# Kernel optimization log

Hardware: AMD Instinct MI355X
Metric: run time of the kernel (lower is better)

## Reference

```python
import jax, jax.numpy as jnp
import numpy as np

B, S, I, H = 32, 2048, 256, 256


def setup_inputs() -> dict:
    key = jax.random.key(0)
    ks = jax.random.split(key, 12)
    scale = 1.0 / np.sqrt(H + I)  # torch Linear default init scale-ish
    def w(k):
        return jax.random.normal(k, (H + I, H), dtype=jnp.float32) * scale
    def b(k):
        return jax.random.normal(k, (H,), dtype=jnp.float32) * scale
    return {
        "x": jax.random.normal(ks[0], (B, S, I), dtype=jnp.float32),
        "h0": jax.random.normal(ks[1], (1, B, H), dtype=jnp.float32),
        "c0": jax.random.normal(ks[2], (1, B, H), dtype=jnp.float32),
        "Wf": w(ks[3]), "bf": b(ks[4]),
        "Wi": w(ks[5]), "bi": b(ks[6]),
        "Wc": w(ks[7]), "bc": b(ks[8]),
        "Wo": w(ks[9]), "bo": b(ks[10]),
    }


def reference(x, h0, c0, Wf, bf, Wi, bi, Wc, bc, Wo, bo):
    # Fuse the four gate GEMMs into one: W_all [H+I, 4H], b_all [4H]
    W_all = jnp.concatenate([Wf, Wi, Wc, Wo], axis=1)
    b_all = jnp.concatenate([bf, bi, bc, bo], axis=0)
    Hh = h0.shape[-1]

    def step(carry, x_t):
        h, c = carry  # [B,H]
        hx = jnp.concatenate([h, x_t], axis=-1)          # [B, H+I]
        g = hx @ W_all + b_all                            # [B, 4H]
        f = jax.nn.sigmoid(g[:, 0*Hh:1*Hh])
        i = jax.nn.sigmoid(g[:, 1*Hh:2*Hh])
        cand = jnp.tanh(g[:, 2*Hh:3*Hh])
        o = jax.nn.sigmoid(g[:, 3*Hh:4*Hh])
        c_new = c * f + i * cand
        h_new = o * jnp.tanh(c_new)
        return (h_new, c_new), h_new

    (h_f, c_f), hs = jax.lax.scan(step, (h0[0], c0[0]), jnp.swapaxes(x, 0, 1))
    hidden_states = jnp.swapaxes(hs, 0, 1)               # [B,S,H]
    return hidden_states, (h_f[None], c_f[None])
```

## Files before the change

### kernel.cpp

```cpp
#include <hip/hip_runtime.h>
#include <hip/hip_bf16.h>

typedef __attribute__((ext_vector_type(8))) short short8;
typedef __attribute__((ext_vector_type(4))) float floatx4;
typedef __attribute__((ext_vector_type(4))) unsigned int uintx4;
typedef unsigned int u32;

#define Bb 32
#define Ss 2048
#define Ii 256
#define Hh 256

#define DATA_OFF 4096
#define GX_OFF   65536
#define RETRY_DEAD (1u << 22)

__device__ __forceinline__ unsigned short f2bf(float f) {
    unsigned int u = __float_as_uint(f);
    u += 0x7fffu + ((u >> 16) & 1u);
    return (unsigned short)(u >> 16);
}
__device__ __forceinline__ float bf2f_lo(u32 w) { return __uint_as_float(w << 16); }
__device__ __forceinline__ float bf2f_hi(u32 w) { return __uint_as_float(w & 0xffff0000u); }

__device__ __forceinline__ float fast_sigmoid(float x) {
    return __builtin_amdgcn_rcpf(1.0f + __expf(-x));
}
__device__ __forceinline__ float fast_tanh(float x) {
    return 1.0f - 2.0f * __builtin_amdgcn_rcpf(__expf(2.0f * x) + 1.0f);
}

__device__ __forceinline__ void data_load8_s(const u32* pd, uintx4 v[8]) {
    asm volatile("global_load_dwordx4 %0, %8, off sc0 sc1\n\t"
                 "global_load_dwordx4 %1, %8, off offset:64 sc0 sc1\n\t"
                 "global_load_dwordx4 %2, %8, off offset:128 sc0 sc1\n\t"
                 "global_load_dwordx4 %3, %8, off offset:192 sc0 sc1\n\t"
                 "global_load_dwordx4 %4, %8, off offset:256 sc0 sc1\n\t"
                 "global_load_dwordx4 %5, %8, off offset:320 sc0 sc1\n\t"
                 "global_load_dwordx4 %6, %8, off offset:384 sc0 sc1\n\t"
                 "global_load_dwordx4 %7, %8, off offset:448 sc0 sc1\n\t"
                 "s_waitcnt vmcnt(0)"
                 : "=v"(v[0]), "=v"(v[1]), "=v"(v[2]), "=v"(v[3]),
                   "=v"(v[4]), "=v"(v[5]), "=v"(v[6]), "=v"(v[7])
                 : "v"(pd) : "memory");
}

__global__ __launch_bounds__(256, 2)
void lstm_gx_kernel(const float* __restrict__ x,
                    const float* __restrict__ Wf, const float* __restrict__ bfp,
                    const float* __restrict__ Wi, const float* __restrict__ bip,
                    const float* __restrict__ Wc, const float* __restrict__ bcp,
                    const float* __restrict__ Wo, const float* __restrict__ bop,
                    u32* __restrict__ gx)
{
    const int tid = threadIdx.x, wave = tid >> 6, lane = tid & 63;
    const int ln = lane & 15, lg = lane >> 4;
    const int combo = blockIdx.x & 7;
    const int tbase = (blockIdx.x >> 3) * 8;
    const int wg = ((combo & 1) << 2) + wave;
    const int chalf = (combo >> 1) & 1, mtile = combo >> 2;
    const int j0 = wg * 32 + chalf * 16, r0 = mtile * 16;
    const int wv = wg * 4 + chalf * 2 + mtile;

    const float* Wg[4] = {Wf, Wi, Wc, Wo};
    const float* bg[4] = {bfp, bip, bcp, bop};
    float bias[4];
#pragma unroll
    for (int g = 0; g < 4; ++g) bias[g] = bg[g][j0 + ln];

    short8 Bf[4][8];
#pragma unroll
    for (int g = 0; g < 4; ++g)
#pragma unroll
        for (int ks = 0; ks < 8; ++ks) {
            short8 v;
#pragma unroll
            for (int i = 0; i < 8; ++i) {
                int k = 256 + 32 * ks + 8 * lg + i;
                v[i] = (short)f2bf(Wg[g][k * Hh + (j0 + ln)]);
            }
            Bf[g][ks] = v;
        }

    for (int it = 0; it < 8; ++it) {
        int t = tbase + it;
        short8 xf[8];
#pragma unroll
        for (int ks = 0; ks < 8; ++ks) {
            const float* px = x + (r0 + ln) * (Ss * Ii) + t * Ii + 32 * ks + 8 * lg;
            floatx4 a = *(const floatx4*)px;
            floatx4 b = *(const floatx4*)(px + 4);
            short8 v;
#pragma unroll
            for (int q = 0; q < 4; ++q) { v[q] = (short)f2bf(a[q]); v[4 + q] = (short)f2bf(b[q]); }
            xf[ks] = v;
        }
        floatx4 acc[4];
#pragma unroll
        for (int g = 0; g < 4; ++g) acc[g] = (floatx4){0.f, 0.f, 0.f, 0.f};
#pragma unroll
        for (int ks = 0; ks < 8; ++ks)
#pragma unroll
            for (int g = 0; g < 4; ++g)
                acc[g] = __builtin_amdgcn_mfma_f32_16x16x32_bf16(xf[ks], Bf[g][ks], acc[g], 0, 0, 0);

        u32 o[8];
#pragma unroll
        for (int g = 0; g < 4; ++g)
#pragma unroll
            for (int rp = 0; rp < 2; ++rp) {
                float v0 = acc[g][2 * rp] + bias[g];
                float v1 = acc[g][2 * rp + 1] + bias[g];
                o[g * 2 + rp] = (u32)f2bf(v0) | ((u32)f2bf(v1) << 16);
            }
        u32* dst = gx + ((size_t)(t * 32 + wv) * 64 + lane) * 8;
        ((uintx4*)dst)[0] = (uintx4){o[0], o[1], o[2], o[3]};
        ((uintx4*)dst)[1] = (uintx4){o[4], o[5], o[6], o[7]};
    }
}

__global__ __launch_bounds__(256, 1)
void lstm_rec8(const float* __restrict__ h0,
               const float* __restrict__ c0,
               const float* __restrict__ Wf,
               const float* __restrict__ Wi,
               const float* __restrict__ Wc,
               const float* __restrict__ Wo,
               float* __restrict__ out,
               u32* data, const u32* __restrict__ gx)
{
    const int wg = blockIdx.x;
    const int tid = threadIdx.x;
    const int wave = tid >> 6, lane = tid & 63;
    const int mt = wave & 1, chalf = wave >> 1;
    const int ln = lane & 15, lg = lane >> 4;
    const int j0 = wg * 32 + chalf * 16;
    const int j = j0 + ln;
    const int wv = wg * 4 + chalf * 2 + mt;

    const float* Wg[4] = {Wf, Wi, Wc, Wo};
    short8 Bfrag[4][8];
#pragma unroll
    for (int g = 0; g < 4; ++g)
#pragma unroll
        for (int ks = 0; ks < 8; ++ks) {
            short8 v;
#pragma unroll
            for (int i = 0; i < 8; ++i) {
                int k = 32 * ks + 8 * lg + i;
                v[i] = (short)f2bf(Wg[g][k * Hh + j]);
            }
            Bfrag[g][ks] = v;
        }

    float cst[4], hl[4];
#pragma unroll
    for (int r = 0; r < 4; ++r) {
        cst[r] = c0[(16 * mt + 4 * lg + r) * Hh + j];
        hl[r] = 0.0f;
    }

    auto step_tail = [&](floatx4 (&acc)[4], int t, int sw_) {
        float hnew[4];
#pragma unroll
        for (int r = 0; r < 4; ++r) {
            float fg = fast_sigmoid(acc[0][r]);
            float ig = fast_sigmoid(acc[1][r]);
            float cd = fast_tanh(acc[2][r]);
            float og = fast_sigmoid(acc[3][r]);
            float c  = cst[r] * fg + ig * cd;
            cst[r] = c;
            hnew[r] = og * fast_tanh(c);
            hl[r] = hnew[r];
        }
        const u32 tb = 0x4000u | ((u32)(t & 1) << 30);
        u32 wrd[4];
#pragma unroll
        for (int r = 0; r < 4; ++r) {
            float partner = __shfl_xor(hnew[r], 1);
            wrd[r] = ((u32)f2bf(hnew[r]) | ((u32)f2bf(partner) << 16)) | tb;
        }
        u32* pw = data + sw_ * 4096 + (16 * mt + 4 * lg) * 128 + (j >> 1);
        if ((ln & 1) == 0) {
            asm volatile("global_store_dword %4, %0, off sc0 sc1\n\t"
                         "global_store_dword %4, %1, off offset:512 sc0 sc1\n\t"
                         "global_store_dword %4, %2, off offset:1024 sc0 sc1\n\t"
                         "global_store_dword %4, %3, off offset:1536 sc0 sc1"
                         :: "v"(wrd[0]), "v"(wrd[1]), "v"(wrd[2]), "v"(wrd[3]), "v"(pw)
                         : "memory");
        }
#pragma unroll
        for (int r = 0; r < 4; ++r)
            out[(16 * mt + 4 * lg + r) * (Ss * Hh) + t * Hh + j] = hnew[r];
    };

    auto run_mfma = [&](short8 (&afr)[8], floatx4 (&acc)[4]) {
#pragma unroll
        for (int ks = 0; ks < 8; ++ks)
#pragma unroll
            for (int g = 0; g < 4; ++g)
                acc[g] = __builtin_amdgcn_mfma_f32_16x16x32_bf16(afr[ks], Bfrag[g][ks], acc[g], 0, 0, 0);
    };

    uintx4 g0, g1;
    {
        const uintx4* p = (const uintx4*)(gx + ((size_t)wv * 64 + lane) * 8);
        g0 = p[0]; g1 = p[1];
    }

    {
        short8 a0[8];
        const float* hr = h0 + (16 * mt + ln) * Hh;
#pragma unroll
        for (int ks = 0; ks < 8; ++ks) {
            floatx4 a = *(const floatx4*)(hr + 32 * ks + 8 * lg);
            floatx4 b = *(const floatx4*)(hr + 32 * ks + 8 * lg + 4);
            short8 v;
#pragma unroll
            for (int q = 0; q < 4; ++q) { v[q] = (short)f2bf(a[q]); v[4 + q] = (short)f2bf(b[q]); }
            a0[ks] = v;
        }
        floatx4 acc[4];
        acc[0] = (floatx4){bf2f_lo(g0.x), bf2f_hi(g0.x), bf2f_lo(g0.y), bf2f_hi(g0.y)};
        acc[1] = (floatx4){bf2f_lo(g0.z), bf2f_hi(g0.z), bf2f_lo(g0.w), bf2f_hi(g0.w)};
        acc[2] = (floatx4){bf2f_lo(g1.x), bf2f_hi(g1.x), bf2f_lo(g1.y), bf2f_hi(g1.y)};
        acc[3] = (floatx4){bf2f_lo(g1.z), bf2f_hi(g1.z), bf2f_lo(g1.w), bf2f_hi(g1.w)};
        {
            const uintx4* pn = (const uintx4*)(gx + ((size_t)(1 * 32 + wv) * 64 + lane) * 8);
            g0 = pn[0]; g1 = pn[1];
        }
        run_mfma(a0, acc);
        step_tail(acc, 0, 0);
    }

    int sr = 0, sw = 1;
    for (int t = 1; t < Ss; ++t) {
        const u32 want = 0x4000u | ((u32)((t - 1) & 1) << 30);
        const u32* pd = data + sr * 4096 + (16 * mt + ln) * 128 + 4 * lg;
        uintx4 dv[8];
        {
            u32 it = 0;
            for (;;) {
                data_load8_s(pd, dv);
                u32 bad = 0;
#pragma unroll
                for (int ks = 0; ks < 8; ++ks) {
                    bad |= (dv[ks].x & 0x40004000u) ^ want;
                    bad |= (dv[ks].y & 0x40004000u) ^ want;
                    bad |= (dv[ks].z & 0x40004000u) ^ want;
                    bad |= (dv[ks].w & 0x40004000u) ^ want;
                }
                if (!__any((int)(bad != 0))) break;
                if (++it >= RETRY_DEAD) break;
            }
        }
        short8 afr[8];
#pragma unroll
        for (int ks = 0; ks < 8; ++ks) {
            union { uintx4 u; short8 s; } cv;
            cv.u = (uintx4){dv[ks].x & 0xBFFFBFFFu, dv[ks].y & 0xBFFFBFFFu,
                            dv[ks].z & 0xBFFFBFFFu, dv[ks].w & 0xBFFFBFFFu};
            afr[ks] = cv.s;
        }

        floatx4 acc[4];
        acc[0] = (floatx4){bf2f_lo(g0.x), bf2f_hi(g0.x), bf2f_lo(g0.y), bf2f_hi(g0.y)};
        acc[1] = (floatx4){bf2f_lo(g0.z), bf2f_hi(g0.z), bf2f_lo(g0.w), bf2f_hi(g0.w)};
        acc[2] = (floatx4){bf2f_lo(g1.x), bf2f_hi(g1.x), bf2f_lo(g1.y), bf2f_hi(g1.y)};
        acc[3] = (floatx4){bf2f_lo(g1.z), bf2f_hi(g1.z), bf2f_lo(g1.w), bf2f_hi(g1.w)};
        if (t + 1 < Ss) {
            const uintx4* pn = (const uintx4*)(gx + ((size_t)((t + 1) * 32 + wv) * 64 + lane) * 8);
            g0 = pn[0]; g1 = pn[1];
        }

        run_mfma(afr, acc);
        step_tail(acc, t, sw);

        sr = sw; sw = (sw == 2) ? 0 : sw + 1;
    }

    float* hfo = out + Bb * Ss * Hh;
    float* cfo = hfo + Bb * Hh;
#pragma unroll
    for (int r = 0; r < 4; ++r) {
        int b = 16 * mt + 4 * lg + r;
        hfo[b * Hh + j] = hl[r];
        cfo[b * Hh + j] = cst[r];
    }
}

extern "C" void kernel_launch(void* const* d_in, const int* in_sizes, int n_in,
                              void* d_out, int out_size, void* d_ws, size_t ws_size,
                              hipStream_t stream) {
    (void)in_sizes; (void)n_in; (void)out_size; (void)ws_size;
    const float* x  = (const float*)d_in[0];
    const float* h0 = (const float*)d_in[1];
    const float* c0 = (const float*)d_in[2];
    const float* Wf = (const float*)d_in[3]; const float* bf = (const float*)d_in[4];
    const float* Wi = (const float*)d_in[5]; const float* bi = (const float*)d_in[6];
    const float* Wc = (const float*)d_in[7]; const float* bc = (const float*)d_in[8];
    const float* Wo = (const float*)d_in[9]; const float* bo = (const float*)d_in[10];

    u32* data = (u32*)((char*)d_ws + DATA_OFF);
    u32* gx   = (u32*)((char*)d_ws + GX_OFF);

    hipMemsetAsync(d_ws, 0, 65536, stream);

    hipLaunchKernelGGL(lstm_gx_kernel, dim3(2048), dim3(256), 0, stream,
                       x, Wf, bf, Wi, bi, Wc, bc, Wo, bo, gx);
    hipLaunchKernelGGL(lstm_rec8, dim3(8), dim3(256), 0, stream,
                       h0, c0, Wf, Wi, Wc, Wo, (float*)d_out, data, gx);
}
```

Measured before the change: 6.216 ms.

## Prefetch input-gate projections in 4-step windows with nontemporal loads in recurrent loop

Unrolls the recurrent time loop by 8 and prefetches precomputed input-gate projections four timesteps ahead using double-buffered register windows issued via inline asm nontemporal loads. The goal is to hide global-memory latency for the gx reads behind the per-step spin-wait and MFMA work instead of prefetching one step ahead. It also adds a sticky dead flag and lowers the retry limit, so a stuck poll skips all later waits. The cost is more live registers and unrolled code size, with some risk of spills.

```diff
diff --git a/kernel.cpp b/kernel.cpp
--- a/kernel.cpp
+++ b/kernel.cpp
@@ -13,7 +13,7 @@
 
 #define DATA_OFF 4096
 #define GX_OFF   65536
-#define RETRY_DEAD (1u << 22)
+#define RETRY_DEAD (1u << 17)
 
 __device__ __forceinline__ unsigned short f2bf(float f) {
     unsigned int u = __float_as_uint(f);
@@ -119,15 +119,68 @@
     }
 }
 
+#define ISSUE_WIN(A0,A1,B0,B1,C0,C1,D0,D1, Q0,Q1,Q2,Q3)                          \
+    asm volatile("global_load_dwordx4 %0, %8, off nt\n\t"                         \
+                 "global_load_dwordx4 %1, %8, off offset:16 nt\n\t"               \
+                 "global_load_dwordx4 %2, %9, off nt\n\t"                         \
+                 "global_load_dwordx4 %3, %9, off offset:16 nt\n\t"               \
+                 "global_load_dwordx4 %4, %10, off nt\n\t"                        \
+                 "global_load_dwordx4 %5, %10, off offset:16 nt\n\t"              \
+                 "global_load_dwordx4 %6, %11, off nt\n\t"                        \
+                 "global_load_dwordx4 %7, %11, off offset:16 nt"                  \
+                 : "=&v"(A0), "=&v"(A1), "=&v"(B0), "=&v"(B1),                    \
+                   "=&v"(C0), "=&v"(C1), "=&v"(D0), "=&v"(D1)                     \
+                 : "v"(Q0), "v"(Q1), "v"(Q2), "v"(Q3) : "memory")
+
+#define POLL_STEP(T_) do {                                                        \
+    const u32 want_ = 0x4000u | ((u32)(((T_) - 1) & 1) << 30);                    \
+    const u32* pd_ = data + sr * 4096 + (16 * mt + ln) * 128 + 4 * lg;            \
+    u32 it_ = 0;                                                                  \
+    for (;;) {                                                                    \
+        data_load8_s(pd_, dv);                                                    \
+        if (dead) break;                                                          \
+        u32 bad_ = 0;                                                             \
+        _Pragma("unroll")                                                         \
+        for (int ks = 0; ks < 8; ++ks) {                                          \
+            bad_ |= (dv[ks].x & 0x40004000u) ^ want_;                             \
+            bad_ |= (dv[ks].y & 0x40004000u) ^ want_;                             \
+            bad_ |= (dv[ks].z & 0x40004000u) ^ want_;                             \
+            bad_ |= (dv[ks].w & 0x40004000u) ^ want_;                             \
+        }                                                                         \
+        if (!__any((int)(bad_ != 0))) break;                                      \
+        if (++it_ >= RETRY_DEAD) { dead = 1u; break; }                            \
+    }                                                                             \
+    __builtin_amdgcn_sched_barrier(0);                                            \
+} while (0)
+
+#define STEP_BODY(T_, GA_, GB_) do {                                              \
+    short8 afr_[8];                                                               \
+    _Pragma("unroll")                                                             \
+    for (int ks = 0; ks < 8; ++ks) {                                              \
+        union { uintx4 u; short8 s; } cv_;                                        \
+        cv_.u = (uintx4){dv[ks].x & 0xBFFFBFFFu, dv[ks].y & 0xBFFFBFFFu,          \
+                         dv[ks].z & 0xBFFFBFFFu, dv[ks].w & 0xBFFFBFFFu};         \
+        afr_[ks] = cv_.s;                                                         \
+    }                                                                             \
+    floatx4 acc_[4];                                                              \
+    acc_[0] = (floatx4){bf2f_lo(GA_.x), bf2f_hi(GA_.x), bf2f_lo(GA_.y), bf2f_hi(GA_.y)}; \
+    acc_[1] = (floatx4){bf2f_lo(GA_.z), bf2f_hi(GA_.z), bf2f_lo(GA_.w), bf2f_hi(GA_.w)}; \
+    acc_[2] = (floatx4){bf2f_lo(GB_.x), bf2f_hi(GB_.x), bf2f_lo(GB_.y), bf2f_hi(GB_.y)}; \
+    acc_[3] = (floatx4){bf2f_lo(GB_.z), bf2f_hi(GB_.z), bf2f_lo(GB_.w), bf2f_hi(GB_.w)}; \
+    run_mfma(afr_, acc_);                                                         \
+    step_tail(acc_, (T_), sw);                                                    \
+    sr = sw; sw = (sw == 2) ? 0 : sw + 1;                                         \
+} while (0)
+
 __global__ __launch_bounds__(256, 1)
-void lstm_rec8(const float* __restrict__ h0,
-               const float* __restrict__ c0,
-               const float* __restrict__ Wf,
-               const float* __restrict__ Wi,
-               const float* __restrict__ Wc,
-               const float* __restrict__ Wo,
-               float* __restrict__ out,
-               u32* data, const u32* __restrict__ gx)
+void lstm_rec10(const float* __restrict__ h0,
+                const float* __restrict__ c0,
+                const float* __restrict__ Wf,
+                const float* __restrict__ Wi,
+                const float* __restrict__ Wc,
+                const float* __restrict__ Wo,
+                float* __restrict__ out,
+                u32* data, const u32* __restrict__ gx)
 {
     const int wg = blockIdx.x;
     const int tid = threadIdx.x;
@@ -202,10 +255,18 @@
                 acc[g] = __builtin_amdgcn_mfma_f32_16x16x32_bf16(afr[ks], Bfrag[g][ks], acc[g], 0, 0, 0);
     };
 
-    uintx4 g0, g1;
+    uintx4 dv[8];
+    u32 dead = 0;
+
+    uintx4 wA0, wA1, wB0, wB1, wC0, wC1, wD0, wD1;
+    uintx4 nA0, nA1, nB0, nB1, nC0, nC1, nD0, nD1;
+
     {
-        const uintx4* p = (const uintx4*)(gx + ((size_t)wv * 64 + lane) * 8);
-        g0 = p[0]; g1 = p[1];
+        const uintx4* p;
+        p = (const uintx4*)(gx + ((size_t)(1 * 32 + wv) * 64 + lane) * 8); wA0 = p[0]; wA1 = p[1];
+        p = (const uintx4*)(gx + ((size_t)(2 * 32 + wv) * 64 + lane) * 8); wB0 = p[0]; wB1 = p[1];
+        p = (const uintx4*)(gx + ((size_t)(3 * 32 + wv) * 64 + lane) * 8); wC0 = p[0]; wC1 = p[1];
+        p = (const uintx4*)(gx + ((size_t)(4 * 32 + wv) * 64 + lane) * 8); wD0 = p[0]; wD1 = p[1];
     }
 
     {
@@ -220,63 +281,50 @@
             for (int q = 0; q < 4; ++q) { v[q] = (short)f2bf(a[q]); v[4 + q] = (short)f2bf(b[q]); }
             a0[ks] = v;
         }
+        const uintx4* p = (const uintx4*)(gx + ((size_t)wv * 64 + lane) * 8);
+        uintx4 g0 = p[0], g1 = p[1];
         floatx4 acc[4];
         acc[0] = (floatx4){bf2f_lo(g0.x), bf2f_hi(g0.x), bf2f_lo(g0.y), bf2f_hi(g0.y)};
         acc[1] = (floatx4){bf2f_lo(g0.z), bf2f_hi(g0.z), bf2f_lo(g0.w), bf2f_hi(g0.w)};
         acc[2] = (floatx4){bf2f_lo(g1.x), bf2f_hi(g1.x), bf2f_lo(g1.y), bf2f_hi(g1.y)};
         acc[3] = (floatx4){bf2f_lo(g1.z), bf2f_hi(g1.z), bf2f_lo(g1.w), bf2f_hi(g1.w)};
-        {
-            const uintx4* pn = (const uintx4*)(gx + ((size_t)(1 * 32 + wv) * 64 + lane) * 8);
-            g0 = pn[0]; g1 = pn[1];
-        }
         run_mfma(a0, acc);
         step_tail(acc, 0, 0);
     }
 
     int sr = 0, sw = 1;
-    for (int t = 1; t < Ss; ++t) {
-        const u32 want = 0x4000u | ((u32)((t - 1) & 1) << 30);
-        const u32* pd = data + sr * 4096 + (16 * mt + ln) * 128 + 4 * lg;
-        uintx4 dv[8];
+
+    for (int tb = 1; tb <= 2033; tb += 8) {
+        POLL_STEP(tb);
         {
-            u32 it = 0;
-            for (;;) {
-                data_load8_s(pd, dv);
-                u32 bad = 0;
-#pragma unroll
-                for (int ks = 0; ks < 8; ++ks) {
-                    bad |= (dv[ks].x & 0x40004000u) ^ want;
-                    bad |= (dv[ks].y & 0x40004000u) ^ want;
-                    bad |= (dv[ks].z & 0x40004000u) ^ want;
-                    bad |= (dv[ks].w & 0x40004000u) ^ want;
-                }
-                if (!__any((int)(bad != 0))) break;
-                if (++it >= RETRY_DEAD) break;
-            }
-        }
-        short8 afr[8];
-#pragma unroll
-        for (int ks = 0; ks < 8; ++ks) {
-            union { uintx4 u; short8 s; } cv;
-            cv.u = (uintx4){dv[ks].x & 0xBFFFBFFFu, dv[ks].y & 0xBFFFBFFFu,
-                            dv[ks].z & 0xBFFFBFFFu, dv[ks].w & 0xBFFFBFFFu};
-            afr[ks] = cv.s;
-        }
-
-        floatx4 acc[4];
-        acc[0] = (floatx4){bf2f_lo(g0.x), bf2f_hi(g0.x), bf2f_lo(g0.y), bf2f_hi(g0.y)};
-        acc[1] = (floatx4){bf2f_lo(g0.z), bf2f_hi(g0.z), bf2f_lo(g0.w), bf2f_hi(g0.w)};
-        acc[2] = (floatx4){bf2f_lo(g1.x), bf2f_hi(g1.x), bf2f_lo(g1.y), bf2f_hi(g1.y)};
-        acc[3] = (floatx4){bf2f_lo(g1.z), bf2f_hi(g1.z), bf2f_lo(g1.w), bf2f_hi(g1.w)};
-        if (t + 1 < Ss) {
-            const uintx4* pn = (const uintx4*)(gx + ((size_t)((t + 1) * 32 + wv) * 64 + lane) * 8);
-            g0 = pn[0]; g1 = pn[1];
-        }
-
-        run_mfma(afr, acc);
-        step_tail(acc, t, sw);
-
-        sr = sw; sw = (sw == 2) ? 0 : sw + 1;
+            const u32* q0 = gx + ((size_t)((tb + 4) * 32 + wv) * 64 + lane) * 8;
+            ISSUE_WIN(nA0, nA1, nB0, nB1, nC0, nC1, nD0, nD1,
+                      q0, q0 + 16384, q0 + 32768, q0 + 49152);
+        }
+        STEP_BODY(tb, wA0, wA1);
+        POLL_STEP(tb + 1); STEP_BODY(tb + 1, wB0, wB1);
+        POLL_STEP(tb + 2); STEP_BODY(tb + 2, wC0, wC1);
+        POLL_STEP(tb + 3); STEP_BODY(tb + 3, wD0, wD1);
+        POLL_STEP(tb + 4);
+        {
+            const u32* q0 = gx + ((size_t)((tb + 8) * 32 + wv) * 64 + lane) * 8;
+            ISSUE_WIN(wA0, wA1, wB0, wB1, wC0, wC1, wD0, wD1,
+                      q0, q0 + 16384, q0 + 32768, q0 + 49152);
+        }
+        STEP_BODY(tb + 4, nA0, nA1);
+        POLL_STEP(tb + 5); STEP_BODY(tb + 5, nB0, nB1);
+        POLL_STEP(tb + 6); STEP_BODY(tb + 6, nC0, nC1);
+        POLL_STEP(tb + 7); STEP_BODY(tb + 7, nD0, nD1);
+    }
+
+    POLL_STEP(2041); STEP_BODY(2041, wA0, wA1);
+    POLL_STEP(2042); STEP_BODY(2042, wB0, wB1);
+    POLL_STEP(2043); STEP_BODY(2043, wC0, wC1);
+    POLL_STEP(2044); STEP_BODY(2044, wD0, wD1);
+    for (int t = 2045; t < Ss; ++t) {
+        const uintx4* p = (const uintx4*)(gx + ((size_t)(t * 32 + wv) * 64 + lane) * 8);
+        uintx4 ga = p[0], gb = p[1];
+        POLL_STEP(t); STEP_BODY(t, ga, gb);
     }
 
     float* hfo = out + Bb * Ss * Hh;
@@ -308,6 +356,6 @@
 
     hipLaunchKernelGGL(lstm_gx_kernel, dim3(2048), dim3(256), 0, stream,
                        x, Wf, bf, Wi, bi, Wc, bc, Wo, bo, gx);
-    hipLaunchKernelGGL(lstm_rec8, dim3(8), dim3(256), 0, stream,
+    hipLaunchKernelGGL(lstm_rec10, dim3(8), dim3(256), 0, stream,
                        h0, c0, Wf, Wi, Wc, Wo, (float*)d_out, data, gx);
 }
```

After: 7.202 ms. 1.16x slower.

## Issue speculative double-buffered flag polling loads right after publishing h

Applied to the files above, without the earlier changes.

The recurrent kernel now issues two batches of polling loads for the next step's h-exchange buffer, plus the next gx prefetch, at the end of each step instead of at the top of the next. It then checks the first batch, falls back to the second, and only then enters an alternating ping-pong retry loop. This is meant to hide global-memory round-trip latency in the cross-workgroup spin-wait that dominates each timestep. The cost is extra memory traffic and more registers held for the second batch. The deadlock fallback now latches permanently, and its timeout is shorter.

```diff
diff --git a/kernel.cpp b/kernel.cpp
--- a/kernel.cpp
+++ b/kernel.cpp
@@ -13,7 +13,7 @@
 
 #define DATA_OFF 4096
 #define GX_OFF   65536
-#define RETRY_DEAD (1u << 22)
+#define RETRY_DEAD (1u << 17)
 
 __device__ __forceinline__ unsigned short f2bf(float f) {
     unsigned int u = __float_as_uint(f);
@@ -30,20 +30,26 @@
     return 1.0f - 2.0f * __builtin_amdgcn_rcpf(__expf(2.0f * x) + 1.0f);
 }
 
-__device__ __forceinline__ void data_load8_s(const u32* pd, uintx4 v[8]) {
-    asm volatile("global_load_dwordx4 %0, %8, off sc0 sc1\n\t"
-                 "global_load_dwordx4 %1, %8, off offset:64 sc0 sc1\n\t"
-                 "global_load_dwordx4 %2, %8, off offset:128 sc0 sc1\n\t"
-                 "global_load_dwordx4 %3, %8, off offset:192 sc0 sc1\n\t"
-                 "global_load_dwordx4 %4, %8, off offset:256 sc0 sc1\n\t"
-                 "global_load_dwordx4 %5, %8, off offset:320 sc0 sc1\n\t"
-                 "global_load_dwordx4 %6, %8, off offset:384 sc0 sc1\n\t"
-                 "global_load_dwordx4 %7, %8, off offset:448 sc0 sc1\n\t"
-                 "s_waitcnt vmcnt(0)"
-                 : "=v"(v[0]), "=v"(v[1]), "=v"(v[2]), "=v"(v[3]),
-                   "=v"(v[4]), "=v"(v[5]), "=v"(v[6]), "=v"(v[7])
-                 : "v"(pd) : "memory");
-}
+#define WAITV(N) do { asm volatile("s_waitcnt vmcnt(" #N ")" ::: "memory"); \
+                      __builtin_amdgcn_sched_barrier(0); } while (0)
+
+#define ISSUE8(V, PD)                                                        \
+    asm volatile("global_load_dwordx4 %0, %8, off sc0 sc1\n\t"               \
+                 "global_load_dwordx4 %1, %8, off offset:64 sc0 sc1\n\t"     \
+                 "global_load_dwordx4 %2, %8, off offset:128 sc0 sc1\n\t"    \
+                 "global_load_dwordx4 %3, %8, off offset:192 sc0 sc1\n\t"    \
+                 "global_load_dwordx4 %4, %8, off offset:256 sc0 sc1\n\t"    \
+                 "global_load_dwordx4 %5, %8, off offset:320 sc0 sc1\n\t"    \
+                 "global_load_dwordx4 %6, %8, off offset:384 sc0 sc1\n\t"    \
+                 "global_load_dwordx4 %7, %8, off offset:448 sc0 sc1"        \
+                 : "=&v"(V[0]), "=&v"(V[1]), "=&v"(V[2]), "=&v"(V[3]),       \
+                   "=&v"(V[4]), "=&v"(V[5]), "=&v"(V[6]), "=&v"(V[7])        \
+                 : "v"(PD) : "memory")
+
+#define ISSUEG(GA, GB, P)                                                    \
+    asm volatile("global_load_dwordx4 %0, %2, off\n\t"                       \
+                 "global_load_dwordx4 %1, %2, off offset:16"                 \
+                 : "=&v"(GA), "=&v"(GB) : "v"(P) : "memory")
 
 __global__ __launch_bounds__(256, 2)
 void lstm_gx_kernel(const float* __restrict__ x,
@@ -120,14 +126,14 @@
 }
 
 __global__ __launch_bounds__(256, 1)
-void lstm_rec8(const float* __restrict__ h0,
-               const float* __restrict__ c0,
-               const float* __restrict__ Wf,
-               const float* __restrict__ Wi,
-               const float* __restrict__ Wc,
-               const float* __restrict__ Wo,
-               float* __restrict__ out,
-               u32* data, const u32* __restrict__ gx)
+void lstm_rec11(const float* __restrict__ h0,
+                const float* __restrict__ c0,
+                const float* __restrict__ Wf,
+                const float* __restrict__ Wi,
+                const float* __restrict__ Wc,
+                const float* __restrict__ Wo,
+                float* __restrict__ out,
+                u32* data, const u32* __restrict__ gx)
 {
     const int wg = blockIdx.x;
     const int tid = threadIdx.x;
@@ -160,8 +166,23 @@
         hl[r] = 0.0f;
     }
 
-    auto step_tail = [&](floatx4 (&acc)[4], int t, int sw_) {
-        float hnew[4];
+    uintx4 dvA[8], dvB[8];
+    uintx4 g0, g1;
+    u32 itb = 0, dead = 0;
+
+    auto chk = [&](const uintx4 v[8], u32 want) -> bool {
+        u32 bad = 0;
+#pragma unroll
+        for (int ks = 0; ks < 8; ++ks) {
+            bad |= (v[ks].x & 0x40004000u) ^ want;
+            bad |= (v[ks].y & 0x40004000u) ^ want;
+            bad |= (v[ks].z & 0x40004000u) ^ want;
+            bad |= (v[ks].w & 0x40004000u) ^ want;
+        }
+        return !__any((int)(bad != 0));
+    };
+
+    auto gates = [&](floatx4 (&acc)[4], float (&hnew)[4]) {
 #pragma unroll
         for (int r = 0; r < 4; ++r) {
             float fg = fast_sigmoid(acc[0][r]);
@@ -173,6 +194,19 @@
             hnew[r] = og * fast_tanh(c);
             hl[r] = hnew[r];
         }
+    };
+
+    auto run_mfma = [&](short8 (&afr)[8], floatx4 (&acc)[4]) {
+#pragma unroll
+        for (int ks = 0; ks < 8; ++ks)
+#pragma unroll
+            for (int g = 0; g < 4; ++g)
+                acc[g] = __builtin_amdgcn_mfma_f32_16x16x32_bf16(afr[ks], Bfrag[g][ks], acc[g], 0, 0, 0);
+    };
+
+    int sr = 0, sw = 0;
+
+    auto tail = [&](int t, const float hnew[4]) {
         const u32 tb = 0x4000u | ((u32)(t & 1) << 30);
         u32 wrd[4];
 #pragma unroll
@@ -180,7 +214,7 @@
             float partner = __shfl_xor(hnew[r], 1);
             wrd[r] = ((u32)f2bf(hnew[r]) | ((u32)f2bf(partner) << 16)) | tb;
         }
-        u32* pw = data + sw_ * 4096 + (16 * mt + 4 * lg) * 128 + (j >> 1);
+        u32* pw = data + sw * 4096 + (16 * mt + 4 * lg) * 128 + (j >> 1);
         if ((ln & 1) == 0) {
             asm volatile("global_store_dword %4, %0, off sc0 sc1\n\t"
                          "global_store_dword %4, %1, off offset:512 sc0 sc1\n\t"
@@ -192,21 +226,14 @@
 #pragma unroll
         for (int r = 0; r < 4; ++r)
             out[(16 * mt + 4 * lg + r) * (Ss * Hh) + t * Hh + j] = hnew[r];
+        const u32* pdn = data + sw * 4096 + (16 * mt + ln) * 128 + 4 * lg;
+        ISSUE8(dvA, pdn);
+        ISSUE8(dvB, pdn);
+        int tg = (t + 1 < Ss) ? (t + 1) : (Ss - 1);
+        const u32* pg = gx + ((size_t)(tg * 32 + wv) * 64 + lane) * 8;
+        ISSUEG(g0, g1, pg);
+        sr = sw; sw = (sw == 2) ? 0 : sw + 1;
     };
-
-    auto run_mfma = [&](short8 (&afr)[8], floatx4 (&acc)[4]) {
-#pragma unroll
-        for (int ks = 0; ks < 8; ++ks)
-#pragma unroll
-            for (int g = 0; g < 4; ++g)
-                acc[g] = __builtin_amdgcn_mfma_f32_16x16x32_bf16(afr[ks], Bfrag[g][ks], acc[g], 0, 0, 0);
-    };
-
-    uintx4 g0, g1;
-    {
-        const uintx4* p = (const uintx4*)(gx + ((size_t)wv * 64 + lane) * 8);
-        g0 = p[0]; g1 = p[1];
-    }
 
     {
         short8 a0[8];
@@ -219,64 +246,68 @@
 #pragma unroll
             for (int q = 0; q < 4; ++q) { v[q] = (short)f2bf(a[q]); v[4 + q] = (short)f2bf(b[q]); }
             a0[ks] = v;
+        }
+        const uintx4* p = (const uintx4*)(gx + ((size_t)wv * 64 + lane) * 8);
+        uintx4 ga = p[0], gb = p[1];
+        floatx4 acc[4];
+        acc[0] = (floatx4){bf2f_lo(ga.x), bf2f_hi(ga.x), bf2f_lo(ga.y), bf2f_hi(ga.y)};
+        acc[1] = (floatx4){bf2f_lo(ga.z), bf2f_hi(ga.z), bf2f_lo(ga.w), bf2f_hi(ga.w)};
+        acc[2] = (floatx4){bf2f_lo(gb.x), bf2f_hi(gb.x), bf2f_lo(gb.y), bf2f_hi(gb.y)};
+        acc[3] = (floatx4){bf2f_lo(gb.z), bf2f_hi(gb.z), bf2f_lo(gb.w), bf2f_hi(gb.w)};
+        run_mfma(a0, acc);
+        float hnew[4];
+        gates(acc, hnew);
+        tail(0, hnew);
+    }
+
+    for (int t = 1; t < Ss; ++t) {
+        const u32 want = 0x4000u | ((u32)((t - 1) & 1) << 30);
+        const u32* pdc = data + sr * 4096 + (16 * mt + ln) * 128 + 4 * lg;
+
+        int have = 0;
+        WAITV(10);
+        if (dead || chk(dvA, want)) have = 1;
+        else {
+            WAITV(2);
+            if (chk(dvB, want)) have = 2;
+        }
+        if (!have) {
+            ISSUE8(dvA, pdc); ISSUE8(dvB, pdc);
+            WAITV(8);
+            if (chk(dvA, want)) have = 1;
+            while (!have) {
+                ISSUE8(dvA, pdc);
+                WAITV(8);
+                if (chk(dvB, want)) { have = 2; break; }
+                ISSUE8(dvB, pdc);
+                WAITV(8);
+                if (chk(dvA, want)) { have = 1; break; }
+                if (++itb >= RETRY_DEAD) { dead = 1; have = 1; }
+            }
+        }
+        WAITV(0);
+        if (have == 2) {
+#pragma unroll
+            for (int ks = 0; ks < 8; ++ks) dvA[ks] = dvB[ks];
+        }
+
+        short8 afr[8];
+#pragma unroll
+        for (int ks = 0; ks < 8; ++ks) {
+            union { uintx4 u; short8 s; } cv;
+            cv.u = (uintx4){dvA[ks].x & 0xBFFFBFFFu, dvA[ks].y & 0xBFFFBFFFu,
+                            dvA[ks].z & 0xBFFFBFFFu, dvA[ks].w & 0xBFFFBFFFu};
+            afr[ks] = cv.s;
         }
         floatx4 acc[4];
         acc[0] = (floatx4){bf2f_lo(g0.x), bf2f_hi(g0.x), bf2f_lo(g0.y), bf2f_hi(g0.y)};
         acc[1] = (floatx4){bf2f_lo(g0.z), bf2f_hi(g0.z), bf2f_lo(g0.w), bf2f_hi(g0.w)};
         acc[2] = (floatx4){bf2f_lo(g1.x), bf2f_hi(g1.x), bf2f_lo(g1.y), bf2f_hi(g1.y)};
         acc[3] = (floatx4){bf2f_lo(g1.z), bf2f_hi(g1.z), bf2f_lo(g1.w), bf2f_hi(g1.w)};
-        {
-            const uintx4* pn = (const uintx4*)(gx + ((size_t)(1 * 32 + wv) * 64 + lane) * 8);
-            g0 = pn[0]; g1 = pn[1];
-        }
-        run_mfma(a0, acc);
-        step_tail(acc, 0, 0);
-    }
-
-    int sr = 0, sw = 1;
-    for (int t = 1; t < Ss; ++t) {
-        const u32 want = 0x4000u | ((u32)((t - 1) & 1) << 30);
-        const u32* pd = data + sr * 4096 + (16 * mt + ln) * 128 + 4 * lg;
-        uintx4 dv[8];
-        {
-            u32 it = 0;
-            for (;;) {
-                data_load8_s(pd, dv);
-                u32 bad = 0;
-#pragma unroll
-                for (int ks = 0; ks < 8; ++ks) {
-                    bad |= (dv[ks].x & 0x40004000u) ^ want;
-                    bad |= (dv[ks].y & 0x40004000u) ^ want;
-                    bad |= (dv[ks].z & 0x40004000u) ^ want;
-                    bad |= (dv[ks].w & 0x40004000u) ^ want;
-                }
-                if (!__any((int)(bad != 0))) break;
-                if (++it >= RETRY_DEAD) break;
-            }
-        }
-        short8 afr[8];
-#pragma unroll
-        for (int ks = 0; ks < 8; ++ks) {
-            union { uintx4 u; short8 s; } cv;
-            cv.u = (uintx4){dv[ks].x & 0xBFFFBFFFu, dv[ks].y & 0xBFFFBFFFu,
-                            dv[ks].z & 0xBFFFBFFFu, dv[ks].w & 0xBFFFBFFFu};
-            afr[ks] = cv.s;
-        }
-
-        floatx4 acc[4];
-        acc[0] = (floatx4){bf2f_lo(g0.x), bf2f_hi(g0.x), bf2f_lo(g0.y), bf2f_hi(g0.y)};
-        acc[1] = (floatx4){bf2f_lo(g0.z), bf2f_hi(g0.z), bf2f_lo(g0.w), bf2f_hi(g0.w)};
-        acc[2] = (floatx4){bf2f_lo(g1.x), bf2f_hi(g1.x), bf2f_lo(g1.y), bf2f_hi(g1.y)};
-        acc[3] = (floatx4){bf2f_lo(g1.z), bf2f_hi(g1.z), bf2f_lo(g1.w), bf2f_hi(g1.w)};
-        if (t + 1 < Ss) {
-            const uintx4* pn = (const uintx4*)(gx + ((size_t)((t + 1) * 32 + wv) * 64 + lane) * 8);
-            g0 = pn[0]; g1 = pn[1];
-        }
-
         run_mfma(afr, acc);
-        step_tail(acc, t, sw);
-
-        sr = sw; sw = (sw == 2) ? 0 : sw + 1;
+        float hnew[4];
+        gates(acc, hnew);
+        tail(t, hnew);
     }
 
     float* hfo = out + Bb * Ss * Hh;
@@ -308,6 +339,6 @@
 
     hipLaunchKernelGGL(lstm_gx_kernel, dim3(2048), dim3(256), 0, stream,
                        x, Wf, bf, Wi, bi, Wc, bc, Wo, bo, gx);
-    hipLaunchKernelGGL(lstm_rec8, dim3(8), dim3(256), 0, stream,
+    hipLaunchKernelGGL(lstm_rec11, dim3(8), dim3(256), 0, stream,
                        h0, c0, Wf, Wi, Wc, Wo, (float*)d_out, data, gx);
 }
```

After: 8.234 ms. +32.5%, slower.
